# Optimization experiments

Hardware: AMD Instinct MI355X
Metric: run time of the kernel (lower is better)

The kernel has to match this reference:

```python
import jax, jax.numpy as jnp
import numpy as np

N, C, K, H = 131072, 512, 128, 8  # points, channels, patch_size, heads


def setup_inputs() -> dict:
    key = jax.random.key(0)
    ks = jax.random.split(key, 6)
    feat = jax.random.normal(ks[0], (N, C), dtype=jnp.float32)
    Wqkv = jax.random.normal(ks[1], (C, 3 * C), dtype=jnp.float32) * 0.02
    bqkv = jax.random.normal(ks[2], (3 * C,), dtype=jnp.float32) * 0.02
    Wproj = jax.random.normal(ks[3], (C, C), dtype=jnp.float32) * 0.02
    bproj = jax.random.normal(ks[4], (C,), dtype=jnp.float32) * 0.02
    order = jax.random.permutation(ks[5], N).astype(jnp.int64)  # serialized order (all clusters full)
    inverse = jnp.argsort(order).astype(jnp.int64)              # serialized inverse
    return {"feat": feat, "Wqkv": Wqkv, "bqkv": bqkv, "Wproj": Wproj,
            "bproj": bproj, "order": order, "inverse": inverse}


def reference(feat, Wqkv, bqkv, Wproj, bproj, order, inverse):
    hd = C // H
    scale = hd ** -0.5
    qkv = feat @ Wqkv + bqkv                 # [N, 3C]
    qkv = qkv[order]                         # gather by serialized order
    qkv = qkv.reshape(-1, K, 3, H, hd)       # [W, K, 3, H, hd]
    qkv = jnp.moveaxis(qkv, 2, 0)            # [3, W, K, H, hd]
    q = jnp.swapaxes(qkv[0], 1, 2)           # [W, H, K, hd]
    k = jnp.swapaxes(qkv[1], 1, 2)
    v = jnp.swapaxes(qkv[2], 1, 2)
    # upcast_attention / upcast_softmax -> compute scores & softmax in fp32
    attn = jnp.einsum('whkd,whjd->whkj', (q * scale).astype(jnp.float32),
                      k.astype(jnp.float32))             # [W, H, K, K]
    attn = jax.nn.softmax(attn, axis=-1).astype(feat.dtype)
    out = jnp.einsum('whkj,whjd->whkd', attn, v)          # [W, H, K, hd]
    out = jnp.swapaxes(out, 1, 2).reshape(-1, C)          # [N, C]
    out = out[inverse]                                    # scatter back via inverse
    out = out @ Wproj + bproj
    return out
```

## Files before the change

kernel.cpp:

```cpp
#include <hip/hip_runtime.h>
#include <hip/hip_bf16.h>
#include <cstdint>
#include <cstddef>

typedef __bf16 bf16;
typedef __bf16 bf16x8 __attribute__((ext_vector_type(8)));
typedef float f32x4 __attribute__((ext_vector_type(4)));

#define N_PTS 131072
#define CDIM  512
#define C3    1536
#define HD    64
#define NH    8
#define KWIN  128

static __device__ __forceinline__ bf16 cvt(float x) { return (bf16)x; }

static __device__ __forceinline__ void gld16(const bf16* g, bf16* l) {
    __builtin_amdgcn_global_load_lds(
        (const __attribute__((address_space(1))) void*)g,
        (__attribute__((address_space(3))) void*)l, 16, 0, 0);
}

__global__ __launch_bounds__(256) void k_prep(
    const float* __restrict__ Wqkv, const float* __restrict__ Wproj,
    bf16* __restrict__ Wqkv_t, bf16* __restrict__ Wproj_t)
{
    int idx = blockIdx.x * 256 + threadIdx.x;
    if (idx < CDIM * C3) {
        int k = idx / C3, c = idx % C3;
        Wqkv_t[(size_t)c * CDIM + k] = cvt(Wqkv[idx]);
    } else {
        int j = idx - CDIM * C3;
        if (j < CDIM * CDIM) {
            int k = j / CDIM, c = j % CDIM;
            Wproj_t[(size_t)c * CDIM + k] = cvt(Wproj[j]);
        }
    }
}

__global__ __launch_bounds__(256) void k_gather(
    const float* __restrict__ feat, const int* __restrict__ order,
    bf16* __restrict__ feat_g)
{
    int row = blockIdx.x * 2 + (threadIdx.x >> 7);
    int c   = (threadIdx.x & 127) << 2;
    int src = order[row];
    float4 v = *reinterpret_cast<const float4*>(feat + (size_t)src * CDIM + c);
    union { bf16 e[4]; uint2 u; } pk;
    pk.e[0] = cvt(v.x); pk.e[1] = cvt(v.y); pk.e[2] = cvt(v.z); pk.e[3] = cvt(v.w);
    *reinterpret_cast<uint2*>(feat_g + (size_t)row * CDIM + c) = pk.u;
}

template <bool F32OUT, int NT>
__global__ __launch_bounds__(512, 2) void k_gemm(
    const bf16* __restrict__ Ag, const bf16* __restrict__ Bt,
    const float* __restrict__ bias, void* __restrict__ outp)
{
    __shared__ __align__(16) bf16 As[3][256 * 32];
    __shared__ __align__(16) bf16 Bs[3][256 * 32];

    const int t    = threadIdx.x;
    const int lane = t & 63;
    const int wv   = t >> 6;
    const int wr   = wv >> 2;
    const int wc   = wv & 3;
    const int g    = lane >> 4, r16 = lane & 15;

    const int nwg = gridDim.x;
    const int bid = blockIdx.x;
    const int swz = (bid & 7) * (nwg >> 3) + (bid >> 3);
    const int m0  = (swz / NT) * 256;
    const int n0  = (swz % NT) * 256;

    const int L0 = wv * 64 + lane;
    const int r0 = L0 >> 2,        s0 = ((L0 & 3) - (r0 >> 1)) & 3;
    const int r1 = r0 + 128,       s1 = ((L0 & 3) - (r1 >> 1)) & 3;
    const bf16* srcA0 = Ag + (size_t)(m0 + r0) * CDIM + s0 * 8;
    const bf16* srcA1 = Ag + (size_t)(m0 + r1) * CDIM + s1 * 8;
    const bf16* srcB0 = Bt + (size_t)(n0 + r0) * CDIM + s0 * 8;
    const bf16* srcB1 = Bt + (size_t)(n0 + r1) * CDIM + s1 * 8;

    int aoff[8], boff[4];
#pragma unroll
    for (int i = 0; i < 8; ++i) {
        int row = wr * 128 + i * 16 + r16;
        aoff[i] = row * 64 + (((g + (row >> 1)) & 3) << 4);
    }
#pragma unroll
    for (int n = 0; n < 4; ++n) {
        int row = wc * 64 + n * 16 + r16;
        boff[n] = row * 64 + (((g + (row >> 1)) & 3) << 4);
    }

    f32x4 acc[8][4];
    const f32x4 z = {0.f, 0.f, 0.f, 0.f};
#pragma unroll
    for (int i = 0; i < 8; ++i)
#pragma unroll
        for (int n = 0; n < 4; ++n) acc[i][n] = z;

    const int NKT = CDIM / 32;

    auto stageA = [&](int s) {
        const int b  = s % 3;
        const int ko = s * 32;
        gld16(srcA0 + ko, &As[b][(size_t)wv * 64 * 8]);
        gld16(srcA1 + ko, &As[b][(size_t)(512 + wv * 64) * 8]);
    };
    auto stageB = [&](int s) {
        const int b  = s % 3;
        const int ko = s * 32;
        gld16(srcB0 + ko, &Bs[b][(size_t)wv * 64 * 8]);
        gld16(srcB1 + ko, &Bs[b][(size_t)(512 + wv * 64) * 8]);
    };

    stageA(0); stageB(0); stageA(1); stageB(1);
    asm volatile("s_waitcnt vmcnt(4)" ::: "memory");
    __builtin_amdgcn_s_barrier();
    __builtin_amdgcn_sched_barrier(0);

#pragma unroll
    for (int s = 0; s < NKT; ++s) {
        const int b = s % 3;
        const char* abase = reinterpret_cast<const char*>(&As[b][0]);
        const char* bbase = reinterpret_cast<const char*>(&Bs[b][0]);

        bf16x8 af0[4], bv[4];
#pragma unroll
        for (int i = 0; i < 4; ++i)
            af0[i] = *reinterpret_cast<const bf16x8*>(abase + aoff[i]);
#pragma unroll
        for (int n = 0; n < 4; ++n)
            bv[n] = *reinterpret_cast<const bf16x8*>(bbase + boff[n]);
        if (s < NKT - 2) stageA(s + 2);
        __builtin_amdgcn_s_barrier();
        asm volatile("s_waitcnt lgkmcnt(0)" ::: "memory");
        __builtin_amdgcn_sched_barrier(0);
        __builtin_amdgcn_s_setprio(1);
#pragma unroll
        for (int i = 0; i < 4; ++i)
#pragma unroll
            for (int n = 0; n < 4; ++n)
                acc[i][n] = __builtin_amdgcn_mfma_f32_16x16x32_bf16(
                    af0[i], bv[n], acc[i][n], 0, 0, 0);
        __builtin_amdgcn_s_setprio(0);
        __builtin_amdgcn_s_barrier();
        __builtin_amdgcn_sched_barrier(0);

        bf16x8 af1[4];
#pragma unroll
        for (int i = 0; i < 4; ++i)
            af1[i] = *reinterpret_cast<const bf16x8*>(abase + aoff[4 + i]);
        if (s < NKT - 2) stageB(s + 2);
        __builtin_amdgcn_s_barrier();
        asm volatile("s_waitcnt lgkmcnt(0)" ::: "memory");
        __builtin_amdgcn_sched_barrier(0);
        __builtin_amdgcn_s_setprio(1);
#pragma unroll
        for (int i = 0; i < 4; ++i)
#pragma unroll
            for (int n = 0; n < 4; ++n)
                acc[4 + i][n] = __builtin_amdgcn_mfma_f32_16x16x32_bf16(
                    af1[i], bv[n], acc[4 + i][n], 0, 0, 0);
        __builtin_amdgcn_s_setprio(0);
        if (s < NKT - 2)
            asm volatile("s_waitcnt vmcnt(4)" ::: "memory");
        else if (s == NKT - 2)
            asm volatile("s_waitcnt vmcnt(0)" ::: "memory");
        __builtin_amdgcn_s_barrier();
        __builtin_amdgcn_sched_barrier(0);
    }

    const int ldo = NT * 256;
#pragma unroll
    for (int n = 0; n < 4; ++n) {
        int col = n0 + wc * 64 + n * 16 + r16;
        float b = bias[col];
#pragma unroll
        for (int i = 0; i < 8; ++i)
#pragma unroll
            for (int j = 0; j < 4; ++j) {
                int row = m0 + wr * 128 + i * 16 + g * 4 + j;
                if (F32OUT)
                    reinterpret_cast<float*>(outp)[(size_t)row * ldo + col] =
                        acc[i][n][j] + b;
                else
                    reinterpret_cast<bf16*>(outp)[(size_t)row * ldo + col] =
                        cvt(acc[i][n][j] + b);
            }
    }
}

__global__ __launch_bounds__(256) void k_attn(
    const bf16* __restrict__ qkv_s, const int* __restrict__ order,
    bf16* __restrict__ attn_g)
{
    __shared__ __align__(16) char smem[36864 + 64 * 136 * 2];
    __shared__ int ord_s[KWIN];
    bf16 (*Q)[72]   = reinterpret_cast<bf16 (*)[72]>(smem);
    bf16 (*Kt)[72]  = reinterpret_cast<bf16 (*)[72]>(smem + 128 * 72 * 2);
    bf16 (*P)[136]  = reinterpret_cast<bf16 (*)[136]>(smem);
    bf16 (*Vt)[136] = reinterpret_cast<bf16 (*)[136]>(smem + 36864);

    const int t    = threadIdx.x;
    const int lane = t & 63;
    const int wv   = t >> 6;
    const int g    = lane >> 4, r16 = lane & 15;
    const int h    = blockIdx.x;
    const int w    = blockIdx.y;

    const bf16* base = qkv_s + (size_t)w * KWIN * C3 + h * HD;

    if (t < KWIN) ord_s[t] = order[w * KWIN + t];

#pragma unroll
    for (int it = 0; it < 4; ++it) {
        int s   = it * 256 + t;
        int tok = s >> 3;
        int c8  = (s & 7) << 3;
        size_t roff = (size_t)tok * C3 + c8;
        *reinterpret_cast<uint4*>(&Q[tok][c8])  =
            *reinterpret_cast<const uint4*>(base + roff);
        *reinterpret_cast<uint4*>(&Kt[tok][c8]) =
            *reinterpret_cast<const uint4*>(base + roff + CDIM);
        uint4 vvec = *reinterpret_cast<const uint4*>(base + roff + 2 * CDIM);
        const bf16* ve = reinterpret_cast<const bf16*>(&vvec);
#pragma unroll
        for (int i = 0; i < 8; ++i) Vt[c8 + i][tok] = ve[i];
    }
    __syncthreads();

    f32x4 sc[2][8];
    const f32x4 z = {0.f, 0.f, 0.f, 0.f};
#pragma unroll
    for (int m = 0; m < 2; ++m)
#pragma unroll
        for (int n = 0; n < 8; ++n) sc[m][n] = z;

#pragma unroll
    for (int ks = 0; ks < 2; ++ks) {
        bf16x8 aq[2];
#pragma unroll
        for (int m = 0; m < 2; ++m)
            aq[m] = *reinterpret_cast<const bf16x8*>(
                &Q[wv * 32 + m * 16 + r16][ks * 32 + g * 8]);
#pragma unroll
        for (int n = 0; n < 8; ++n) {
            bf16x8 bk = *reinterpret_cast<const bf16x8*>(
                &Kt[n * 16 + r16][ks * 32 + g * 8]);
#pragma unroll
            for (int m = 0; m < 2; ++m)
                sc[m][n] = __builtin_amdgcn_mfma_f32_16x16x32_bf16(
                    aq[m], bk, sc[m][n], 0, 0, 0);
        }
    }

    const float scale = 0.125f;
    float inv_sum[2][4];
#pragma unroll
    for (int m = 0; m < 2; ++m) {
#pragma unroll
        for (int j = 0; j < 4; ++j) {
            float mx = -3.0e38f;
#pragma unroll
            for (int n = 0; n < 8; ++n) mx = fmaxf(mx, sc[m][n][j]);
            mx = fmaxf(mx, __shfl_xor(mx, 1));
            mx = fmaxf(mx, __shfl_xor(mx, 2));
            mx = fmaxf(mx, __shfl_xor(mx, 4));
            mx = fmaxf(mx, __shfl_xor(mx, 8));
            mx *= scale;
            float ssum = 0.f;
#pragma unroll
            for (int n = 0; n < 8; ++n) {
                float p = __expf(sc[m][n][j] * scale - mx);
                sc[m][n][j] = p;
                ssum += p;
            }
            ssum += __shfl_xor(ssum, 1);
            ssum += __shfl_xor(ssum, 2);
            ssum += __shfl_xor(ssum, 4);
            ssum += __shfl_xor(ssum, 8);
            inv_sum[m][j] = 1.f / ssum;
        }
    }

    __syncthreads();

#pragma unroll
    for (int m = 0; m < 2; ++m)
#pragma unroll
        for (int n = 0; n < 8; ++n)
#pragma unroll
            for (int j = 0; j < 4; ++j)
                P[wv * 32 + m * 16 + g * 4 + j][n * 16 + r16] =
                    cvt(sc[m][n][j] * inv_sum[m][j]);

    f32x4 o[2][4];
#pragma unroll
    for (int m = 0; m < 2; ++m)
#pragma unroll
        for (int n = 0; n < 4; ++n) o[m][n] = z;

#pragma unroll
    for (int kt = 0; kt < 4; ++kt) {
        bf16x8 ap[2];
#pragma unroll
        for (int m = 0; m < 2; ++m)
            ap[m] = *reinterpret_cast<const bf16x8*>(
                &P[wv * 32 + m * 16 + r16][kt * 32 + g * 8]);
#pragma unroll
        for (int n = 0; n < 4; ++n) {
            bf16x8 bv = *reinterpret_cast<const bf16x8*>(
                &Vt[n * 16 + r16][kt * 32 + g * 8]);
#pragma unroll
            for (int m = 0; m < 2; ++m)
                o[m][n] = __builtin_amdgcn_mfma_f32_16x16x32_bf16(
                    ap[m], bv, o[m][n], 0, 0, 0);
        }
    }

#pragma unroll
    for (int m = 0; m < 2; ++m)
#pragma unroll
        for (int n = 0; n < 4; ++n)
#pragma unroll
            for (int j = 0; j < 4; ++j) {
                int tok  = wv * 32 + m * 16 + g * 4 + j;
                int d    = n * 16 + r16;
                int drow = ord_s[tok];
                attn_g[(size_t)drow * CDIM + h * HD + d] = cvt(o[m][n][j]);
            }
}

extern "C" void kernel_launch(void* const* d_in, const int* in_sizes, int n_in,
                              void* d_out, int out_size, void* d_ws, size_t ws_size,
                              hipStream_t stream)
{
    const float* feat    = (const float*)d_in[0];
    const float* Wqkv    = (const float*)d_in[1];
    const float* bqkv    = (const float*)d_in[2];
    const float* Wproj   = (const float*)d_in[3];
    const float* bproj   = (const float*)d_in[4];
    const int*   order   = (const int*)d_in[5];
    float* out = (float*)d_out;

    const size_t qkv_bytes  = (size_t)N_PTS * C3 * sizeof(bf16);
    const size_t gat_bytes  = (size_t)N_PTS * CDIM * sizeof(bf16);
    const size_t wq_bytes   = (size_t)C3 * CDIM * sizeof(bf16);
    const size_t wp_bytes   = (size_t)CDIM * CDIM * sizeof(bf16);
    if (ws_size < qkv_bytes + gat_bytes + wq_bytes + wp_bytes) return;

    bf16* qkv_s     = (bf16*)d_ws;
    bf16* shared134 = (bf16*)((char*)d_ws + qkv_bytes);
    bf16* Wqkv_t    = (bf16*)((char*)d_ws + qkv_bytes + gat_bytes);
    bf16* Wproj_t   = (bf16*)((char*)d_ws + qkv_bytes + gat_bytes + wq_bytes);

    k_prep<<<dim3((CDIM * C3 + CDIM * CDIM + 255) / 256), 256, 0, stream>>>(
        Wqkv, Wproj, Wqkv_t, Wproj_t);
    k_gather<<<dim3(N_PTS / 2), 256, 0, stream>>>(feat, order, shared134);
    k_gemm<false, C3 / 256><<<dim3((N_PTS / 256) * (C3 / 256)), 512, 0, stream>>>(
        shared134, Wqkv_t, bqkv, qkv_s);
    k_attn<<<dim3(NH, N_PTS / KWIN), 256, 0, stream>>>(qkv_s, order, shared134);
    k_gemm<true, CDIM / 256><<<dim3((N_PTS / 256) * (CDIM / 256)), 512, 0, stream>>>(
        shared134, Wproj_t, bproj, out);
}
```

Before: 640.7 us.

## Fuse row gather and fp32-to-bf16 cast into QKV GEMM, load B from global

Removes the separate gather kernel. The QKV GEMM now reads fp32 feature rows through the permutation, converts them to bf16 in registers and writes them into a double-buffered swizzled LDS tile. B-operand fragments are now loaded directly from global memory into registers, double-buffered across k-steps, instead of being staged through LDS. The main loop is restructured into one MFMA phase per k-step with fewer barriers. This saves a full intermediate bf16 write and read, but it re-reads each gathered fp32 row for every one of the six N tiles and adds register-path loads with conversion latency inside the loop.

```diff
diff --git a/kernel.cpp b/kernel.cpp
--- a/kernel.cpp
+++ b/kernel.cpp
@@ -39,26 +39,14 @@
     }
 }
 
-__global__ __launch_bounds__(256) void k_gather(
-    const float* __restrict__ feat, const int* __restrict__ order,
-    bf16* __restrict__ feat_g)
-{
-    int row = blockIdx.x * 2 + (threadIdx.x >> 7);
-    int c   = (threadIdx.x & 127) << 2;
-    int src = order[row];
-    float4 v = *reinterpret_cast<const float4*>(feat + (size_t)src * CDIM + c);
-    union { bf16 e[4]; uint2 u; } pk;
-    pk.e[0] = cvt(v.x); pk.e[1] = cvt(v.y); pk.e[2] = cvt(v.z); pk.e[3] = cvt(v.w);
-    *reinterpret_cast<uint2*>(feat_g + (size_t)row * CDIM + c) = pk.u;
-}
-
-template <bool F32OUT, int NT>
-__global__ __launch_bounds__(512, 2) void k_gemm(
-    const bf16* __restrict__ Ag, const bf16* __restrict__ Bt,
-    const float* __restrict__ bias, void* __restrict__ outp)
+template <bool GATHER, bool F32OUT, int NT>
+__global__ __launch_bounds__(512) void k_gemm(
+    const void* __restrict__ Ag_, const bf16* __restrict__ Bt,
+    const float* __restrict__ bias, const int* __restrict__ order,
+    void* __restrict__ outp)
 {
     __shared__ __align__(16) bf16 As[3][256 * 32];
-    __shared__ __align__(16) bf16 Bs[3][256 * 32];
+    __shared__ int ord_s[256];
 
     const int t    = threadIdx.x;
     const int lane = t & 63;
@@ -73,25 +61,43 @@
     const int m0  = (swz / NT) * 256;
     const int n0  = (swz % NT) * 256;
 
+    const float* Af = (const float*)Ag_;
+    const bf16*  Ab = (const bf16*)Ag_;
+    const int NKT = CDIM / 32;
+
+    if (GATHER) {
+        if (t < 256) ord_s[t] = order[m0 + t];
+        __syncthreads();
+    }
+
+    size_t gsrc[4]; int gdst[4];
+    if (GATHER) {
+#pragma unroll
+        for (int q = 0; q < 4; ++q) {
+            int c = t + q * 512;
+            int row = c >> 3, k4 = c & 7;
+            gsrc[q] = (size_t)ord_s[row] * CDIM + k4 * 4;
+            gdst[q] = row * 64 + ((((k4 >> 1) + (row >> 1)) & 3) << 4) + (k4 & 1) * 8;
+        }
+    }
+
     const int L0 = wv * 64 + lane;
-    const int r0 = L0 >> 2,        s0 = ((L0 & 3) - (r0 >> 1)) & 3;
-    const int r1 = r0 + 128,       s1 = ((L0 & 3) - (r1 >> 1)) & 3;
-    const bf16* srcA0 = Ag + (size_t)(m0 + r0) * CDIM + s0 * 8;
-    const bf16* srcA1 = Ag + (size_t)(m0 + r1) * CDIM + s1 * 8;
-    const bf16* srcB0 = Bt + (size_t)(n0 + r0) * CDIM + s0 * 8;
-    const bf16* srcB1 = Bt + (size_t)(n0 + r1) * CDIM + s1 * 8;
-
-    int aoff[8], boff[4];
+    const int r0 = L0 >> 2, sl0 = ((L0 & 3) - (r0 >> 1)) & 3;
+    const int r1 = r0 + 128, sl1 = ((L0 & 3) - (r1 >> 1)) & 3;
+    const bf16* srcA0 = Ab + (size_t)(m0 + r0) * CDIM + sl0 * 8;
+    const bf16* srcA1 = Ab + (size_t)(m0 + r1) * CDIM + sl1 * 8;
+
+    const bf16* srcB[4];
+#pragma unroll
+    for (int n = 0; n < 4; ++n)
+        srcB[n] = Bt + (size_t)(n0 + wc * 64 + n * 16 + r16) * CDIM + g * 8;
+
+    int aoff[8];
 #pragma unroll
     for (int i = 0; i < 8; ++i) {
         int row = wr * 128 + i * 16 + r16;
         aoff[i] = row * 64 + (((g + (row >> 1)) & 3) << 4);
     }
-#pragma unroll
-    for (int n = 0; n < 4; ++n) {
-        int row = wc * 64 + n * 16 + r16;
-        boff[n] = row * 64 + (((g + (row >> 1)) & 3) << 4);
-    }
 
     f32x4 acc[8][4];
     const f32x4 z = {0.f, 0.f, 0.f, 0.f};
@@ -100,76 +106,99 @@
 #pragma unroll
         for (int n = 0; n < 4; ++n) acc[i][n] = z;
 
-    const int NKT = CDIM / 32;
-
-    auto stageA = [&](int s) {
+    auto stageA_g16 = [&](int s) {
         const int b  = s % 3;
         const int ko = s * 32;
         gld16(srcA0 + ko, &As[b][(size_t)wv * 64 * 8]);
         gld16(srcA1 + ko, &As[b][(size_t)(512 + wv * 64) * 8]);
     };
-    auto stageB = [&](int s) {
-        const int b  = s % 3;
-        const int ko = s * 32;
-        gld16(srcB0 + ko, &Bs[b][(size_t)wv * 64 * 8]);
-        gld16(srcB1 + ko, &Bs[b][(size_t)(512 + wv * 64) * 8]);
-    };
-
-    stageA(0); stageB(0); stageA(1); stageB(1);
-    asm volatile("s_waitcnt vmcnt(4)" ::: "memory");
-    __builtin_amdgcn_s_barrier();
-    __builtin_amdgcn_sched_barrier(0);
+
+    bf16x8 bv[2][4];
+
+    if (GATHER) {
+        float4 f0[4];
+#pragma unroll
+        for (int q = 0; q < 4; ++q)
+            f0[q] = *reinterpret_cast<const float4*>(Af + gsrc[q]);
+#pragma unroll
+        for (int n = 0; n < 4; ++n)
+            bv[0][n] = *reinterpret_cast<const bf16x8*>(srcB[n]);
+#pragma unroll
+        for (int q = 0; q < 4; ++q) {
+            union { bf16 e[4]; uint2 u; } pk;
+            pk.e[0] = cvt(f0[q].x); pk.e[1] = cvt(f0[q].y);
+            pk.e[2] = cvt(f0[q].z); pk.e[3] = cvt(f0[q].w);
+            *reinterpret_cast<uint2*>(
+                reinterpret_cast<char*>(&As[0][0]) + gdst[q]) = pk.u;
+        }
+        asm volatile("s_waitcnt lgkmcnt(0)" ::: "memory");
+        __builtin_amdgcn_s_barrier();
+    } else {
+        stageA_g16(0); stageA_g16(1);
+#pragma unroll
+        for (int n = 0; n < 4; ++n)
+            bv[0][n] = *reinterpret_cast<const bf16x8*>(srcB[n]);
+        asm volatile("s_waitcnt vmcnt(6)" ::: "memory");
+        __builtin_amdgcn_s_barrier();
+    }
 
 #pragma unroll
     for (int s = 0; s < NKT; ++s) {
-        const int b = s % 3;
-        const char* abase = reinterpret_cast<const char*>(&As[b][0]);
-        const char* bbase = reinterpret_cast<const char*>(&Bs[b][0]);
-
-        bf16x8 af0[4], bv[4];
-#pragma unroll
-        for (int i = 0; i < 4; ++i)
-            af0[i] = *reinterpret_cast<const bf16x8*>(abase + aoff[i]);
-#pragma unroll
-        for (int n = 0; n < 4; ++n)
-            bv[n] = *reinterpret_cast<const bf16x8*>(bbase + boff[n]);
-        if (s < NKT - 2) stageA(s + 2);
-        __builtin_amdgcn_s_barrier();
-        asm volatile("s_waitcnt lgkmcnt(0)" ::: "memory");
-        __builtin_amdgcn_sched_barrier(0);
+        const int rb = GATHER ? (s & 1) : (s % 3);
+        const char* abase = reinterpret_cast<const char*>(&As[rb][0]);
+
+        float4 fA[4];
+        if (GATHER && s < NKT - 1) {
+#pragma unroll
+            for (int q = 0; q < 4; ++q)
+                fA[q] = *reinterpret_cast<const float4*>(
+                    Af + gsrc[q] + (size_t)(s + 1) * 32);
+        }
+        if (!GATHER && s < NKT - 2) stageA_g16(s + 2);
+        if (s < NKT - 1) {
+#pragma unroll
+            for (int n = 0; n < 4; ++n)
+                bv[(s + 1) & 1][n] = *reinterpret_cast<const bf16x8*>(
+                    srcB[n] + (s + 1) * 32);
+        }
+
+        bf16x8 af[8];
+#pragma unroll
+        for (int i = 0; i < 8; ++i)
+            af[i] = *reinterpret_cast<const bf16x8*>(abase + aoff[i]);
+
         __builtin_amdgcn_s_setprio(1);
 #pragma unroll
-        for (int i = 0; i < 4; ++i)
+        for (int i = 0; i < 8; ++i)
 #pragma unroll
             for (int n = 0; n < 4; ++n)
                 acc[i][n] = __builtin_amdgcn_mfma_f32_16x16x32_bf16(
-                    af0[i], bv[n], acc[i][n], 0, 0, 0);
+                    af[i], bv[s & 1][n], acc[i][n], 0, 0, 0);
         __builtin_amdgcn_s_setprio(0);
-        __builtin_amdgcn_s_barrier();
-        __builtin_amdgcn_sched_barrier(0);
-
-        bf16x8 af1[4];
-#pragma unroll
-        for (int i = 0; i < 4; ++i)
-            af1[i] = *reinterpret_cast<const bf16x8*>(abase + aoff[4 + i]);
-        if (s < NKT - 2) stageB(s + 2);
-        __builtin_amdgcn_s_barrier();
-        asm volatile("s_waitcnt lgkmcnt(0)" ::: "memory");
-        __builtin_amdgcn_sched_barrier(0);
-        __builtin_amdgcn_s_setprio(1);
-#pragma unroll
-        for (int i = 0; i < 4; ++i)
-#pragma unroll
-            for (int n = 0; n < 4; ++n)
-                acc[4 + i][n] = __builtin_amdgcn_mfma_f32_16x16x32_bf16(
-                    af1[i], bv[n], acc[4 + i][n], 0, 0, 0);
-        __builtin_amdgcn_s_setprio(0);
-        if (s < NKT - 2)
-            asm volatile("s_waitcnt vmcnt(4)" ::: "memory");
-        else if (s == NKT - 2)
-            asm volatile("s_waitcnt vmcnt(0)" ::: "memory");
-        __builtin_amdgcn_s_barrier();
-        __builtin_amdgcn_sched_barrier(0);
+
+        if (GATHER) {
+            if (s < NKT - 1) {
+                const int wb = (s + 1) & 1;
+#pragma unroll
+                for (int q = 0; q < 4; ++q) {
+                    union { bf16 e[4]; uint2 u; } pk;
+                    pk.e[0] = cvt(fA[q].x); pk.e[1] = cvt(fA[q].y);
+                    pk.e[2] = cvt(fA[q].z); pk.e[3] = cvt(fA[q].w);
+                    *reinterpret_cast<uint2*>(
+                        reinterpret_cast<char*>(&As[wb][0]) + gdst[q]) = pk.u;
+                }
+                asm volatile("s_waitcnt lgkmcnt(0)" ::: "memory");
+                __builtin_amdgcn_s_barrier();
+            }
+        } else {
+            if (s < NKT - 2) {
+                asm volatile("s_waitcnt vmcnt(6)" ::: "memory");
+                __builtin_amdgcn_s_barrier();
+            } else if (s == NKT - 2) {
+                asm volatile("s_waitcnt vmcnt(4)" ::: "memory");
+                __builtin_amdgcn_s_barrier();
+            }
+        }
     }
 
     const int ldo = NT * 256;
@@ -311,12 +340,12 @@
                 &P[wv * 32 + m * 16 + r16][kt * 32 + g * 8]);
 #pragma unroll
         for (int n = 0; n < 4; ++n) {
-            bf16x8 bv = *reinterpret_cast<const bf16x8*>(
+            bf16x8 bvv = *reinterpret_cast<const bf16x8*>(
                 &Vt[n * 16 + r16][kt * 32 + g * 8]);
 #pragma unroll
             for (int m = 0; m < 2; ++m)
                 o[m][n] = __builtin_amdgcn_mfma_f32_16x16x32_bf16(
-                    ap[m], bv, o[m][n], 0, 0, 0);
+                    ap[m], bvv, o[m][n], 0, 0, 0);
         }
     }
 
@@ -351,17 +380,18 @@
     const size_t wp_bytes   = (size_t)CDIM * CDIM * sizeof(bf16);
     if (ws_size < qkv_bytes + gat_bytes + wq_bytes + wp_bytes) return;
 
-    bf16* qkv_s     = (bf16*)d_ws;
-    bf16* shared134 = (bf16*)((char*)d_ws + qkv_bytes);
-    bf16* Wqkv_t    = (bf16*)((char*)d_ws + qkv_bytes + gat_bytes);
-    bf16* Wproj_t   = (bf16*)((char*)d_ws + qkv_bytes + gat_bytes + wq_bytes);
+    bf16* qkv_s   = (bf16*)d_ws;
+    bf16* attn_g  = (bf16*)((char*)d_ws + qkv_bytes);
+    bf16* Wqkv_t  = (bf16*)((char*)d_ws + qkv_bytes + gat_bytes);
+    bf16* Wproj_t = (bf16*)((char*)d_ws + qkv_bytes + gat_bytes + wq_bytes);
 
     k_prep<<<dim3((CDIM * C3 + CDIM * CDIM + 255) / 256), 256, 0, stream>>>(
         Wqkv, Wproj, Wqkv_t, Wproj_t);
-    k_gather<<<dim3(N_PTS / 2), 256, 0, stream>>>(feat, order, shared134);
-    k_gemm<false, C3 / 256><<<dim3((N_PTS / 256) * (C3 / 256)), 512, 0, stream>>>(
-        shared134, Wqkv_t, bqkv, qkv_s);
-    k_attn<<<dim3(NH, N_PTS / KWIN), 256, 0, stream>>>(qkv_s, order, shared134);
-    k_gemm<true, CDIM / 256><<<dim3((N_PTS / 256) * (CDIM / 256)), 512, 0, stream>>>(
-        shared134, Wproj_t, bproj, out);
-}
+    k_gemm<true, false, C3 / 256>
+        <<<dim3((N_PTS / 256) * (C3 / 256)), 512, 0, stream>>>(
+        feat, Wqkv_t, bqkv, order, qkv_s);
+    k_attn<<<dim3(NH, N_PTS / KWIN), 256, 0, stream>>>(qkv_s, order, attn_g);
+    k_gemm<false, true, CDIM / 256>
+        <<<dim3((N_PTS / 256) * (CDIM / 256)), 512, 0, stream>>>(
+        attn_g, Wproj_t, bproj, order, out);
+}
```

Result: slower. 741.1 us (+15.7%).
